# Kernel tuning notes

Measured on AMD Instinct MI355X. Metric: run time of the kernel, lower is better.

The kernel has to match this reference:

```python
import jax, jax.numpy as jnp
import numpy as np

NEG = -1.0e9  # masked_fill value from the original module

def setup_inputs() -> dict:
    key = jax.random.key(0)
    kq, kk, kv, km = jax.random.split(key, 4)
    B, H, S, D = 4, 16, 2048, 64
    Q = jax.random.normal(kq, (B, H, S, D), dtype=jnp.float32)
    K = jax.random.normal(kk, (B, H, S, D), dtype=jnp.float32)
    V = jax.random.normal(kv, (B, H, S, D), dtype=jnp.float32)
    # boolean mask, True = masked out (broadcast over batch and heads)
    mask = jax.random.randint(km, (1, 1, S, S), 0, 2).astype(jnp.bool_)
    return {"Q": Q, "K": K, "V": V, "mask": mask}

def reference(Q, K, V, mask):
    d_k = K.shape[-1]
    scale = 1.0 / jnp.sqrt(jnp.asarray(d_k, dtype=Q.dtype))
    # [B,H,S,S] attention scores
    scores = jnp.einsum("bhqd,bhkd->bhqk", Q, K) * scale
    scores = jnp.where(mask, jnp.asarray(NEG, dtype=scores.dtype), scores)
    weights = jax.nn.softmax(scores, axis=-1)
    # dropout is identity in eval mode (self.training == False)
    return jnp.einsum("bhqk,bhkd->bhqd", weights, V)
```

## Files before the change

kernel.cpp:

```cpp
#include <hip/hip_runtime.h>
#include <stdint.h>

#define SQ 2048
#define DH 64

typedef __attribute__((ext_vector_type(8))) short bf16x8;
typedef __attribute__((ext_vector_type(4))) short bf16x4;
typedef __attribute__((ext_vector_type(4))) float f32x4;

static __device__ __forceinline__ unsigned short f2bf_rne(float x) {
  union { float f; uint32_t u; } v; v.f = x;
  uint32_t u = v.u;
  return (unsigned short)((u + 0x7FFFu + ((u >> 16) & 1u)) >> 16);
}

static __device__ __forceinline__ uint32_t pack_hi(float a, float b) {
  uint32_t au = __float_as_uint(a), bu = __float_as_uint(b);
#if __has_builtin(__builtin_amdgcn_perm)
  return __builtin_amdgcn_perm(bu, au, 0x07060302u);
#else
  return (bu & 0xFFFF0000u) | (au >> 16);
#endif
}

static __device__ __forceinline__ uint32_t pack_sel(float a, float b, uint32_t sel) {
#if __has_builtin(__builtin_amdgcn_perm)
  return __builtin_amdgcn_perm(__float_as_uint(b), __float_as_uint(a), sel);
#else
  uint32_t r = 0;
  uint64_t src = ((uint64_t)__float_as_uint(b) << 32) | __float_as_uint(a);
  for (int i = 0; i < 4; ++i) {
    uint32_t sb = (sel >> (8 * i)) & 0xFF;
    uint32_t byte = (sb < 8) ? (uint32_t)((src >> (8 * sb)) & 0xFF) : 0u;
    r |= byte << (8 * i);
  }
  return r;
#endif
}

static __device__ __forceinline__ float fast_exp2(float x) {
#if __has_builtin(__builtin_amdgcn_exp2f)
  return __builtin_amdgcn_exp2f(x);
#else
  return exp2f(x);
#endif
}

#if __has_builtin(__builtin_amdgcn_mfma_f32_16x16x16_bf16)
#define MFMA_PV(a, b, c) __builtin_amdgcn_mfma_f32_16x16x16_bf16((a), (b), (c), 0, 0, 0)
#else
#define MFMA_PV(a, b, c) __builtin_amdgcn_mfma_f32_16x16x16bf16_1k((a), (b), (c), 0, 0, 0)
#endif

__global__ __launch_bounds__(256) void pack_all(const float* __restrict__ K,
                                                const float* __restrict__ V,
                                                const int* __restrict__ mask,
                                                uint4* __restrict__ pk,
                                                uint2* __restrict__ pv,
                                                uint2* __restrict__ pm) {
  const int t = threadIdx.x;
  if (blockIdx.x < 2048) {
    __shared__ uint32_t Vw[64][33];
    const int bt = blockIdx.x;
    {
      const float* src = K + (size_t)bt * 64 * DH;
      uint4* dst = pk + (size_t)bt * 512;
#pragma unroll
      for (int j = 0; j < 2; ++j) {
        int i = t + j * 256;
        int kk = i >> 3, cp = i & 7;
        int c = cp ^ (kk & 7);
        const float4* s4 = (const float4*)(src + (size_t)kk * DH + c * 8);
        float4 a = s4[0], b = s4[1];
        uint4 w;
        w.x = pack_hi(a.x, a.y); w.y = pack_hi(a.z, a.w);
        w.z = pack_hi(b.x, b.y); w.w = pack_hi(b.z, b.w);
        dst[i] = w;
      }
    }
    {
      const float* src = V + (size_t)bt * 64 * DH;
#pragma unroll
      for (int half = 0; half < 2; ++half) {
        int kp = (t >> 4) + half * 16;
        int d4 = (t & 15) * 4;
        float4 a = *(const float4*)(src + (size_t)(2 * kp) * DH + d4);
        float4 b = *(const float4*)(src + (size_t)(2 * kp + 1) * DH + d4);
        Vw[d4 + 0][kp] = pack_hi(a.x, b.x);
        Vw[d4 + 1][kp] = pack_hi(a.y, b.y);
        Vw[d4 + 2][kp] = pack_hi(a.z, b.z);
        Vw[d4 + 3][kp] = pack_hi(a.w, b.w);
      }
      __syncthreads();
      uint2* dst = pv + (size_t)bt * 1024;
#pragma unroll
      for (int j = 0; j < 4; ++j) {
        int o = t + j * 256;
        int d = o >> 4, up = o & 15;
        int u = up ^ (d & 15);
        uint2 w;
        w.x = Vw[d][2 * u]; w.y = Vw[d][2 * u + 1];
        dst[o] = w;
      }
    }
  } else {
    __shared__ uint2 Lm[16][17];
    const int bid = blockIdx.x - 2048;
    const int qb = bid >> 5, gb = bid & 31;
    {
      int qq = t >> 4, gg = t & 15;
      int4 m = *(const int4*)(mask + (size_t)(qb * 16 + qq) * SQ + (gb * 64 + gg * 4));
      uint2 w;
      w.x = (m.x ? 0x00000C0Cu : 0x00000302u) | (m.y ? 0x0C0C0000u : 0x07060000u);
      w.y = (m.z ? 0x00000C0Cu : 0x00000302u) | (m.w ? 0x0C0C0000u : 0x07060000u);
      Lm[gg][qq] = w;
    }
    __syncthreads();
    {
      int gg = t >> 4, qq = t & 15;
      pm[(size_t)(gb * 16 + gg) * 2048 + qb * 16 + qq] = Lm[gg][qq];
    }
  }
}

__global__ void pack_mask_kernel(const int* __restrict__ mask,
                                 unsigned long long* __restrict__ bits) {
  const int lane = threadIdx.x & 63;
  const int gw = (blockIdx.x * blockDim.x + threadIdx.x) >> 6;
  const int nw = (gridDim.x * blockDim.x) >> 6;
  for (int w = gw; w < SQ * SQ / 64; w += nw) {
    int v = mask[(size_t)w * 64 + lane];
    unsigned long long b = __ballot(v != 0);
    if (lane == 0) bits[(size_t)(w & 31) * SQ + (w >> 5)] = b;
  }
}

__global__ __launch_bounds__(256, 2) void attn3(
    const uint4* __restrict__ pk, const uint4* __restrict__ pv,
    const uint2* __restrict__ pm, const float* __restrict__ Qg,
    float* __restrict__ Og) {
  __shared__ __align__(16) uint8_t smem[32768];

  const int id = blockIdx.x;
  const int bh = id & 63;
  const int qblk = id >> 6;
  const int t = threadIdx.x;
  const int wave = t >> 6, lane = t & 63, col = lane & 15, quad = lane >> 4;

  const float* Qb = Qg + (size_t)bh * SQ * DH;
  float* Ob = Og + (size_t)bh * SQ * DH;
  const uint4* pkb = pk + (size_t)bh * 32 * 512;
  const uint4* pvb = pv + (size_t)bh * 32 * 512;
  const int q0 = qblk * 256 + wave * 64;

  const float QSCALE = 0.18033688011112042f;
  bf16x8 qf[4][2];
#pragma unroll
  for (int s = 0; s < 4; ++s) {
    int q = q0 + s * 16 + col;
#pragma unroll
    for (int j = 0; j < 2; ++j) {
      const float4* p = (const float4*)(Qb + (size_t)q * DH + j * 32 + quad * 8);
      float4 a = p[0], b = p[1];
      bf16x8 f;
      f[0] = (short)f2bf_rne(a.x * QSCALE); f[1] = (short)f2bf_rne(a.y * QSCALE);
      f[2] = (short)f2bf_rne(a.z * QSCALE); f[3] = (short)f2bf_rne(a.w * QSCALE);
      f[4] = (short)f2bf_rne(b.x * QSCALE); f[5] = (short)f2bf_rne(b.y * QSCALE);
      f[6] = (short)f2bf_rne(b.z * QSCALE); f[7] = (short)f2bf_rne(b.w * QSCALE);
      qf[s][j] = f;
    }
  }

  const unsigned ka0 = col * 128 + ((quad ^ (col & 7)) * 16);
  const unsigned ka1 = col * 128 + (((4 + quad) ^ (col & 7)) * 16);
  unsigned va[4];
#pragma unroll
  for (int kt = 0; kt < 4; ++kt)
    va[kt] = 16384u + col * 128 + (((kt * 4 + quad) ^ col) * 8);
  const unsigned stK = t * 16;
  const unsigned stV = 16384u + t * 16;
  const char* pmt = (const char*)pm + (size_t)(quad * 2048 + q0 + col) * 8;

  f32x4 acc[4][4];
  f32x4 accl[4];
#pragma unroll
  for (int s = 0; s < 4; ++s) {
#pragma unroll
    for (int dt = 0; dt < 4; ++dt)
#pragma unroll
      for (int r = 0; r < 4; ++r) acc[s][dt][r] = 0.0f;
#pragma unroll
    for (int r = 0; r < 4; ++r) accl[s][r] = 0.0f;
  }
  bf16x4 vones;
  vones[0] = (short)0x3F80; vones[1] = (short)0x3F80;
  vones[2] = (short)0x3F80; vones[3] = (short)0x3F80;
  const f32x4 fz = {0.0f, 0.0f, 0.0f, 0.0f};

  {
    uint4 k0 = pkb[t], k1 = pkb[t + 256];
    uint4 v0 = pvb[t], v1 = pvb[t + 256];
    *(uint4*)(smem + stK) = k0; *(uint4*)(smem + stK + 4096) = k1;
    *(uint4*)(smem + stV) = v0; *(uint4*)(smem + stV + 4096) = v1;
  }
  unsigned buf = 0;

  for (int tile = 0; tile < 32; ++tile) {
    __syncthreads();
    const int tn = (tile < 31) ? tile + 1 : 31;

    const uint4* pkt = pkb + (size_t)tn * 512;
    const uint4* pvt = pvb + (size_t)tn * 512;
    uint4 k0 = pkt[t], k1 = pkt[t + 256];
    uint4 v0 = pvt[t], v1 = pvt[t + 256];

#pragma unroll
    for (int kt = 0; kt < 4; ++kt) {
      const bf16x8 kf0 = *(const bf16x8*)(smem + buf + kt * 2048 + ka0);
      const bf16x8 kf1 = *(const bf16x8*)(smem + buf + kt * 2048 + ka1);
      uint2 mw[4];
#pragma unroll
      for (int s = 0; s < 4; ++s)
        mw[s] = *(const uint2*)(pmt + (size_t)kt * 65536 + s * 128);

      uint32_t pf[4][2];
#pragma unroll
      for (int s = 0; s < 4; ++s) {
        f32x4 st = __builtin_amdgcn_mfma_f32_16x16x32_bf16(kf0, qf[s][0], fz, 0, 0, 0);
        st = __builtin_amdgcn_mfma_f32_16x16x32_bf16(kf1, qf[s][1], st, 0, 0, 0);
        float p0 = fast_exp2(st[0]), p1 = fast_exp2(st[1]);
        float p2 = fast_exp2(st[2]), p3 = fast_exp2(st[3]);
        pf[s][0] = pack_sel(p0, p1, mw[s].x);
        pf[s][1] = pack_sel(p2, p3, mw[s].y);
      }

      union { uint2 u2; bf16x4 v; } vf[4];
#pragma unroll
      for (int dt = 0; dt < 4; ++dt)
        vf[dt].u2 = *(const uint2*)(smem + buf + va[kt] + dt * 2048);
#pragma unroll
      for (int s = 0; s < 4; ++s) {
        union { uint32_t u[2]; bf16x4 v; } pw;
        pw.u[0] = pf[s][0]; pw.u[1] = pf[s][1];
        accl[s] = MFMA_PV(vones, pw.v, accl[s]);
#pragma unroll
        for (int dt = 0; dt < 4; ++dt)
          acc[s][dt] = MFMA_PV(vf[dt].v, pw.v, acc[s][dt]);
      }
    }

    const unsigned ob = buf ^ 8192u;
    *(uint4*)(smem + ob + stK) = k0; *(uint4*)(smem + ob + stK + 4096) = k1;
    *(uint4*)(smem + ob + stV) = v0; *(uint4*)(smem + ob + stV + 4096) = v1;
    buf = ob;
    pmt += 262144;
  }

#pragma unroll
  for (int s = 0; s < 4; ++s) {
    float inv = 1.0f / accl[s][0];
    int q = q0 + s * 16 + col;
    float* orow = Ob + (size_t)q * DH;
#pragma unroll
    for (int dt = 0; dt < 4; ++dt) {
      float4 o;
      o.x = acc[s][dt][0] * inv;
      o.y = acc[s][dt][1] * inv;
      o.z = acc[s][dt][2] * inv;
      o.w = acc[s][dt][3] * inv;
      *(float4*)(orow + dt * 16 + quad * 4) = o;
    }
  }
}

__global__ __launch_bounds__(512, 4) void attn_fb(
    const float* __restrict__ Qg, const float* __restrict__ Kg,
    const float* __restrict__ Vg, const unsigned long long* __restrict__ mbits,
    const int* __restrict__ mraw, float* __restrict__ Og) {
  __shared__ __align__(16) unsigned short Klds[2][64][72];
  __shared__ __align__(16) uint32_t Vtlds[2][64][36];
  const int id = blockIdx.x;
  const int bh = id & 63;
  const int qblk = id >> 6;
  const int t = threadIdx.x;
  const int wave = t >> 6, lane = t & 63, col = lane & 15, quad = lane >> 4;
  const float* Qb = Qg + (size_t)bh * SQ * DH;
  const float* Kb = Kg + (size_t)bh * SQ * DH;
  const float* Vb = Vg + (size_t)bh * SQ * DH;
  float* Ob = Og + (size_t)bh * SQ * DH;
  const int q0 = qblk * 256 + wave * 32;
  const int skk = t >> 3, sd8 = (t & 7) * 8, skp = t >> 4, sd4 = (t & 15) * 4;
  const float QSCALE = 0.18033688011112042f;
  bf16x8 qf[2][2];
#pragma unroll
  for (int s = 0; s < 2; ++s) {
    int q = q0 + s * 16 + col;
#pragma unroll
    for (int j = 0; j < 2; ++j) {
      const float4* p = (const float4*)(Qb + (size_t)q * DH + j * 32 + quad * 8);
      float4 a = p[0], b = p[1];
      bf16x8 f;
      f[0] = (short)f2bf_rne(a.x * QSCALE); f[1] = (short)f2bf_rne(a.y * QSCALE);
      f[2] = (short)f2bf_rne(a.z * QSCALE); f[3] = (short)f2bf_rne(a.w * QSCALE);
      f[4] = (short)f2bf_rne(b.x * QSCALE); f[5] = (short)f2bf_rne(b.y * QSCALE);
      f[6] = (short)f2bf_rne(b.z * QSCALE); f[7] = (short)f2bf_rne(b.w * QSCALE);
      qf[s][j] = f;
    }
  }
  f32x4 acc[2][4]; f32x4 accl[2];
#pragma unroll
  for (int s = 0; s < 2; ++s) {
#pragma unroll
    for (int dt = 0; dt < 4; ++dt)
#pragma unroll
      for (int r = 0; r < 4; ++r) acc[s][dt][r] = 0.0f;
#pragma unroll
    for (int r = 0; r < 4; ++r) accl[s][r] = 0.0f;
  }
  bf16x4 vones;
  vones[0] = (short)0x3F80; vones[1] = (short)0x3F80;
  vones[2] = (short)0x3F80; vones[3] = (short)0x3F80;
  const f32x4 fz = {0.0f, 0.0f, 0.0f, 0.0f};
  auto load_mask = [&](int ti, unsigned long long m[2]) {
    if (mbits) {
#pragma unroll
      for (int s = 0; s < 2; ++s)
        m[s] = mbits[(size_t)ti * SQ + (q0 + s * 16 + col)];
    } else {
#pragma unroll
      for (int s = 0; s < 2; ++s) {
        int q = q0 + s * 16 + col;
        unsigned long long mm = 0;
#pragma unroll
        for (int j = 0; j < 4; ++j) {
          int4 mi = *(const int4*)(mraw + (size_t)q * SQ + ti * 64 + j * 16 + quad * 4);
          unsigned long long nib = (unsigned long long)((mi.x != 0) | ((mi.y != 0) << 1) |
                                                        ((mi.z != 0) << 2) | ((mi.w != 0) << 3));
          mm |= nib << (j * 16 + quad * 4);
        }
        m[s] = mm;
      }
    }
  };
  {
    const float4* kp = (const float4*)(Kb + (size_t)skk * DH + sd8);
    float4 k0 = kp[0], k1 = kp[1];
    const float* va = Vb + (size_t)(skp * 2) * DH + sd4;
    float4 v0 = *(const float4*)va, v1 = *(const float4*)(va + DH);
    uint4 kw;
    kw.x = pack_hi(k0.x, k0.y); kw.y = pack_hi(k0.z, k0.w);
    kw.z = pack_hi(k1.x, k1.y); kw.w = pack_hi(k1.z, k1.w);
    *(uint4*)&Klds[0][skk][sd8] = kw;
    Vtlds[0][sd4 + 0][skp] = pack_hi(v0.x, v1.x);
    Vtlds[0][sd4 + 1][skp] = pack_hi(v0.y, v1.y);
    Vtlds[0][sd4 + 2][skp] = pack_hi(v0.z, v1.z);
    Vtlds[0][sd4 + 3][skp] = pack_hi(v0.w, v1.w);
  }
  unsigned long long mcur[2];
  load_mask(0, mcur);
  for (int tile = 0; tile < 32; ++tile) {
    __syncthreads();
    const int cb = tile & 1, nb = cb ^ 1;
    const int tn = (tile + 1 < 32) ? tile + 1 : tile;
    const int kkn = tn * 64;
    const float4* kp = (const float4*)(Kb + (size_t)(kkn + skk) * DH + sd8);
    float4 k0 = kp[0], k1 = kp[1];
    const float* va = Vb + (size_t)(kkn + skp * 2) * DH + sd4;
    float4 v0 = *(const float4*)va;
    float4 v1 = *(const float4*)(va + DH);
    unsigned long long mnxt[2];
    load_mask(tn, mnxt);
    uint32_t pfw[2][4][2];
#pragma unroll
    for (int kt = 0; kt < 4; ++kt) {
      const bf16x8 kf0 = *(const bf16x8*)&Klds[cb][kt * 16 + col][quad * 8];
      const bf16x8 kf1 = *(const bf16x8*)&Klds[cb][kt * 16 + col][32 + quad * 8];
#pragma unroll
      for (int s = 0; s < 2; ++s) {
        f32x4 st = __builtin_amdgcn_mfma_f32_16x16x32_bf16(kf0, qf[s][0], fz, 0, 0, 0);
        st = __builtin_amdgcn_mfma_f32_16x16x32_bf16(kf1, qf[s][1], st, 0, 0, 0);
        uint32_t nib = (uint32_t)(mcur[s] >> (kt * 16 + quad * 4)) & 0xFu;
        float p[4];
#pragma unroll
        for (int r = 0; r < 4; ++r)
          p[r] = fast_exp2(((nib >> r) & 1u) ? -1.0e9f : st[r]);
        pfw[s][kt][0] = pack_hi(p[0], p[1]);
        pfw[s][kt][1] = pack_hi(p[2], p[3]);
      }
    }
    {
      uint4 kw;
      kw.x = pack_hi(k0.x, k0.y); kw.y = pack_hi(k0.z, k0.w);
      kw.z = pack_hi(k1.x, k1.y); kw.w = pack_hi(k1.z, k1.w);
      *(uint4*)&Klds[nb][skk][sd8] = kw;
      Vtlds[nb][sd4 + 0][skp] = pack_hi(v0.x, v1.x);
      Vtlds[nb][sd4 + 1][skp] = pack_hi(v0.y, v1.y);
      Vtlds[nb][sd4 + 2][skp] = pack_hi(v0.z, v1.z);
      Vtlds[nb][sd4 + 3][skp] = pack_hi(v0.w, v1.w);
    }
    mcur[0] = mnxt[0]; mcur[1] = mnxt[1];
#pragma unroll
    for (int kt = 0; kt < 4; ++kt) {
      union { uint32_t u[2]; bf16x4 v; } p0, p1;
      p0.u[0] = pfw[0][kt][0]; p0.u[1] = pfw[0][kt][1];
      p1.u[0] = pfw[1][kt][0]; p1.u[1] = pfw[1][kt][1];
      accl[0] = MFMA_PV(vones, p0.v, accl[0]);
      accl[1] = MFMA_PV(vones, p1.v, accl[1]);
#pragma unroll
      for (int dt = 0; dt < 4; ++dt) {
        union { uint2 u2; bf16x4 v; } cv;
        cv.u2 = *(const uint2*)&Vtlds[cb][dt * 16 + col][kt * 8 + quad * 2];
        acc[0][dt] = MFMA_PV(cv.v, p0.v, acc[0][dt]);
        acc[1][dt] = MFMA_PV(cv.v, p1.v, acc[1][dt]);
      }
    }
  }
#pragma unroll
  for (int s = 0; s < 2; ++s) {
    float inv = 1.0f / accl[s][0];
    int q = q0 + s * 16 + col;
    float* orow = Ob + (size_t)q * DH;
#pragma unroll
    for (int dt = 0; dt < 4; ++dt) {
      float4 o;
      o.x = acc[s][dt][0] * inv;
      o.y = acc[s][dt][1] * inv;
      o.z = acc[s][dt][2] * inv;
      o.w = acc[s][dt][3] * inv;
      *(float4*)(orow + dt * 16 + quad * 4) = o;
    }
  }
}

extern "C" void kernel_launch(void* const* d_in, const int* in_sizes, int n_in,
                              void* d_out, int out_size, void* d_ws, size_t ws_size,
                              hipStream_t stream) {
  const float* Q = (const float*)d_in[0];
  const float* K = (const float*)d_in[1];
  const float* V = (const float*)d_in[2];
  const int* mask = (const int*)d_in[3];
  float* out = (float*)d_out;

  const size_t PK_BYTES = (size_t)64 * 32 * 8192;
  const size_t PV_BYTES = (size_t)64 * 32 * 8192;
  const size_t PM_BYTES = (size_t)512 * 2048 * 8;
  const size_t NEED = PK_BYTES + PV_BYTES + PM_BYTES;

  if (ws_size >= NEED) {
    uint4* pk = (uint4*)d_ws;
    uint2* pv = (uint2*)((char*)d_ws + PK_BYTES);
    uint2* pm = (uint2*)((char*)d_ws + PK_BYTES + PV_BYTES);
    pack_all<<<6144, 256, 0, stream>>>(K, V, mask, pk, pv, pm);
    attn3<<<512, 256, 0, stream>>>(pk, (uint4*)pv, pm, Q, out);
  } else if (ws_size >= (size_t)SQ * SQ / 8) {
    unsigned long long* bits = (unsigned long long*)d_ws;
    pack_mask_kernel<<<1024, 256, 0, stream>>>(mask, bits);
    attn_fb<<<512, 512, 0, stream>>>(Q, K, V, bits, mask, out);
  } else {
    attn_fb<<<512, 512, 0, stream>>>(Q, K, V, nullptr, mask, out);
  }
}
```

Before: 242.7 us.

## Split KV dimension across blocks, use direct global-to-LDS loads and 16x16x32 PV MFMA

The attention kernel now splits the 32 key tiles into two halves, launching 1024 blocks instead of 512. Each block writes unnormalised partial outputs and row sums, and a new norm kernel combines the two halves. K, V and mask packing is re-permuted so the PV product can use the 16x16x32 bf16 MFMA with 8-wide fragments. K/V tiles are staged with global_load_lds instead of going through registers. The split aims at better CU occupancy and latency hiding, at the cost of extra partial-result traffic and a third kernel launch.

```diff
diff --git a/kernel.cpp b/kernel.cpp
--- a/kernel.cpp
+++ b/kernel.cpp
@@ -3,6 +3,7 @@
 
 #define SQ 2048
 #define DH 64
+#define BH 64
 
 typedef __attribute__((ext_vector_type(8))) short bf16x8;
 typedef __attribute__((ext_vector_type(4))) short bf16x4;
@@ -46,17 +47,29 @@
 #endif
 }
 
+#define MFMA32(a, b, c) __builtin_amdgcn_mfma_f32_16x16x32_bf16((a), (b), (c), 0, 0, 0)
 #if __has_builtin(__builtin_amdgcn_mfma_f32_16x16x16_bf16)
-#define MFMA_PV(a, b, c) __builtin_amdgcn_mfma_f32_16x16x16_bf16((a), (b), (c), 0, 0, 0)
+#define MFMA_PV16(a, b, c) __builtin_amdgcn_mfma_f32_16x16x16_bf16((a), (b), (c), 0, 0, 0)
 #else
-#define MFMA_PV(a, b, c) __builtin_amdgcn_mfma_f32_16x16x16bf16_1k((a), (b), (c), 0, 0, 0)
+#define MFMA_PV16(a, b, c) __builtin_amdgcn_mfma_f32_16x16x16bf16_1k((a), (b), (c), 0, 0, 0)
 #endif
+
+static __device__ __forceinline__ void stage16(const uint8_t* g, uint8_t* l) {
+#if __has_builtin(__builtin_amdgcn_global_load_lds)
+  __builtin_amdgcn_global_load_lds(
+      (const __attribute__((address_space(1))) uint32_t*)g,
+      (__attribute__((address_space(3))) uint32_t*)l, 16, 0, 0);
+#else
+  *(uint4*)l = *(const uint4*)g;
+#endif
+}
+
 
 __global__ __launch_bounds__(256) void pack_all(const float* __restrict__ K,
                                                 const float* __restrict__ V,
                                                 const int* __restrict__ mask,
                                                 uint4* __restrict__ pk,
-                                                uint2* __restrict__ pv,
+                                                uint4* __restrict__ pv,
                                                 uint2* __restrict__ pm) {
   const int t = threadIdx.x;
   if (blockIdx.x < 2048) {
@@ -68,9 +81,10 @@
 #pragma unroll
       for (int j = 0; j < 2; ++j) {
         int i = t + j * 256;
-        int kk = i >> 3, cp = i & 7;
-        int c = cp ^ (kk & 7);
-        const float4* s4 = (const float4*)(src + (size_t)kk * DH + c * 8);
+        int p = i >> 3, cp = i & 7;
+        int c = cp ^ (p & 7);
+        int lkk = (p & 0x20) | ((p & 0x0C) << 1) | ((p & 0x10) >> 2) | (p & 3);
+        const float4* s4 = (const float4*)(src + (size_t)lkk * DH + c * 8);
         float4 a = s4[0], b = s4[1];
         uint4 w;
         w.x = pack_hi(a.x, a.y); w.y = pack_hi(a.z, a.w);
@@ -92,14 +106,15 @@
         Vw[d4 + 3][kp] = pack_hi(a.w, b.w);
       }
       __syncthreads();
-      uint2* dst = pv + (size_t)bt * 1024;
-#pragma unroll
-      for (int j = 0; j < 4; ++j) {
+      uint4* dst = pv + (size_t)bt * 512;
+#pragma unroll
+      for (int j = 0; j < 2; ++j) {
         int o = t + j * 256;
-        int d = o >> 4, up = o & 15;
-        int u = up ^ (d & 15);
-        uint2 w;
-        w.x = Vw[d][2 * u]; w.y = Vw[d][2 * u + 1];
+        int d = o >> 3, cp = o & 7;
+        int c = cp ^ (d & 7);
+        uint4 w;
+        w.x = Vw[d][4 * c + 0]; w.y = Vw[d][4 * c + 1];
+        w.z = Vw[d][4 * c + 2]; w.w = Vw[d][4 * c + 3];
         dst[o] = w;
       }
     }
@@ -109,7 +124,8 @@
     const int qb = bid >> 5, gb = bid & 31;
     {
       int qq = t >> 4, gg = t & 15;
-      int4 m = *(const int4*)(mask + (size_t)(qb * 16 + qq) * SQ + (gb * 64 + gg * 4));
+      int off = ((gg >> 3) << 5) | ((gg & 3) << 3) | (gg & 4);
+      int4 m = *(const int4*)(mask + (size_t)(qb * 16 + qq) * SQ + gb * 64 + off);
       uint2 w;
       w.x = (m.x ? 0x00000C0Cu : 0x00000302u) | (m.y ? 0x0C0C0000u : 0x07060000u);
       w.y = (m.z ? 0x00000C0Cu : 0x00000302u) | (m.w ? 0x0C0C0000u : 0x07060000u);
@@ -135,22 +151,23 @@
   }
 }
 
-__global__ __launch_bounds__(256, 2) void attn3(
-    const uint4* __restrict__ pk, const uint4* __restrict__ pv,
+__global__ __launch_bounds__(256, 2) void attn4(
+    const uint8_t* __restrict__ pk, const uint8_t* __restrict__ pv,
     const uint2* __restrict__ pm, const float* __restrict__ Qg,
-    float* __restrict__ Og) {
+    float* __restrict__ opart, float* __restrict__ lpart, int ntiles) {
   __shared__ __align__(16) uint8_t smem[32768];
 
   const int id = blockIdx.x;
   const int bh = id & 63;
-  const int qblk = id >> 6;
+  const int qblk = (id >> 6) & 7;
+  const int split = id >> 9;
+  const int tile0 = split * ntiles;
   const int t = threadIdx.x;
   const int wave = t >> 6, lane = t & 63, col = lane & 15, quad = lane >> 4;
 
   const float* Qb = Qg + (size_t)bh * SQ * DH;
-  float* Ob = Og + (size_t)bh * SQ * DH;
-  const uint4* pkb = pk + (size_t)bh * 32 * 512;
-  const uint4* pvb = pv + (size_t)bh * 32 * 512;
+  const uint8_t* pkb = pk + ((size_t)bh * 32 + tile0) * 8192;
+  const uint8_t* pvb = pv + ((size_t)bh * 32 + tile0) * 8192;
   const int q0 = qblk * 256 + wave * 64;
 
   const float QSCALE = 0.18033688011112042f;
@@ -173,13 +190,13 @@
 
   const unsigned ka0 = col * 128 + ((quad ^ (col & 7)) * 16);
   const unsigned ka1 = col * 128 + (((4 + quad) ^ (col & 7)) * 16);
-  unsigned va[4];
-#pragma unroll
-  for (int kt = 0; kt < 4; ++kt)
-    va[kt] = 16384u + col * 128 + (((kt * 4 + quad) ^ col) * 8);
-  const unsigned stK = t * 16;
-  const unsigned stV = 16384u + t * 16;
-  const char* pmt = (const char*)pm + (size_t)(quad * 2048 + q0 + col) * 8;
+  unsigned va[2];
+#pragma unroll
+  for (int ktp = 0; ktp < 2; ++ktp)
+    va[ktp] = 16384u + col * 128 + (((ktp * 4 + quad) ^ (col & 7)) * 16);
+  const unsigned stOff = (unsigned)t * 16;
+  const char* pmt = (const char*)pm +
+                    ((size_t)(tile0 * 16 + quad) * 2048 + q0 + col) * 8;
 
   f32x4 acc[4][4];
   f32x4 accl[4];
@@ -192,84 +209,117 @@
 #pragma unroll
     for (int r = 0; r < 4; ++r) accl[s][r] = 0.0f;
   }
-  bf16x4 vones;
-  vones[0] = (short)0x3F80; vones[1] = (short)0x3F80;
-  vones[2] = (short)0x3F80; vones[3] = (short)0x3F80;
+  bf16x8 vones8;
+#pragma unroll
+  for (int i = 0; i < 8; ++i) vones8[i] = (short)0x3F80;
   const f32x4 fz = {0.0f, 0.0f, 0.0f, 0.0f};
 
-  {
-    uint4 k0 = pkb[t], k1 = pkb[t + 256];
-    uint4 v0 = pvb[t], v1 = pvb[t + 256];
-    *(uint4*)(smem + stK) = k0; *(uint4*)(smem + stK + 4096) = k1;
-    *(uint4*)(smem + stV) = v0; *(uint4*)(smem + stV + 4096) = v1;
-  }
+  stage16(pkb + stOff, smem + stOff);
+  stage16(pkb + 4096 + stOff, smem + 4096 + stOff);
+  stage16(pvb + stOff, smem + 16384 + stOff);
+  stage16(pvb + 4096 + stOff, smem + 20480 + stOff);
   unsigned buf = 0;
 
-  for (int tile = 0; tile < 32; ++tile) {
+  for (int tt = 0; tt < ntiles; ++tt) {
     __syncthreads();
-    const int tn = (tile < 31) ? tile + 1 : 31;
-
-    const uint4* pkt = pkb + (size_t)tn * 512;
-    const uint4* pvt = pvb + (size_t)tn * 512;
-    uint4 k0 = pkt[t], k1 = pkt[t + 256];
-    uint4 v0 = pvt[t], v1 = pvt[t + 256];
-
-#pragma unroll
-    for (int kt = 0; kt < 4; ++kt) {
-      const bf16x8 kf0 = *(const bf16x8*)(smem + buf + kt * 2048 + ka0);
-      const bf16x8 kf1 = *(const bf16x8*)(smem + buf + kt * 2048 + ka1);
-      uint2 mw[4];
-#pragma unroll
-      for (int s = 0; s < 4; ++s)
-        mw[s] = *(const uint2*)(pmt + (size_t)kt * 65536 + s * 128);
-
-      uint32_t pf[4][2];
+    const int tl = (tt + 1 < ntiles) ? tt + 1 : tt;
+    const uint8_t* pkt = pkb + (size_t)tl * 8192;
+    const uint8_t* pvt = pvb + (size_t)tl * 8192;
+    const unsigned ob = buf ^ 8192u;
+    stage16(pkt + stOff, smem + ob + stOff);
+    stage16(pkt + 4096 + stOff, smem + ob + 4096 + stOff);
+    stage16(pvt + stOff, smem + 16384 + ob + stOff);
+    stage16(pvt + 4096 + stOff, smem + 16384 + ob + 4096 + stOff);
+
+    const char* pmc = pmt + (size_t)tt * 262144;
+#pragma unroll
+    for (int ktp = 0; ktp < 2; ++ktp) {
+      uint32_t pf[4][2][2];
+#pragma unroll
+      for (int kh = 0; kh < 2; ++kh) {
+        const int kt = ktp * 2 + kh;
+        const bf16x8 kf0 = *(const bf16x8*)(smem + buf + kt * 2048 + ka0);
+        const bf16x8 kf1 = *(const bf16x8*)(smem + buf + kt * 2048 + ka1);
+        uint2 mw[4];
+#pragma unroll
+        for (int s = 0; s < 4; ++s)
+          mw[s] = *(const uint2*)(pmc + (size_t)kt * 65536 + s * 128);
+#pragma unroll
+        for (int s = 0; s < 4; ++s) {
+          f32x4 st = MFMA32(kf0, qf[s][0], fz);
+          st = MFMA32(kf1, qf[s][1], st);
+          float p0 = fast_exp2(st[0]), p1 = fast_exp2(st[1]);
+          float p2 = fast_exp2(st[2]), p3 = fast_exp2(st[3]);
+          pf[s][kh][0] = pack_sel(p0, p1, mw[s].x);
+          pf[s][kh][1] = pack_sel(p2, p3, mw[s].y);
+        }
+      }
+      union { uint4 u; bf16x8 v; } vf[4];
+#pragma unroll
+      for (int dt = 0; dt < 4; ++dt)
+        vf[dt].u = *(const uint4*)(smem + buf + dt * 2048 + va[ktp]);
 #pragma unroll
       for (int s = 0; s < 4; ++s) {
-        f32x4 st = __builtin_amdgcn_mfma_f32_16x16x32_bf16(kf0, qf[s][0], fz, 0, 0, 0);
-        st = __builtin_amdgcn_mfma_f32_16x16x32_bf16(kf1, qf[s][1], st, 0, 0, 0);
-        float p0 = fast_exp2(st[0]), p1 = fast_exp2(st[1]);
-        float p2 = fast_exp2(st[2]), p3 = fast_exp2(st[3]);
-        pf[s][0] = pack_sel(p0, p1, mw[s].x);
-        pf[s][1] = pack_sel(p2, p3, mw[s].y);
-      }
-
-      union { uint2 u2; bf16x4 v; } vf[4];
-#pragma unroll
-      for (int dt = 0; dt < 4; ++dt)
-        vf[dt].u2 = *(const uint2*)(smem + buf + va[kt] + dt * 2048);
-#pragma unroll
-      for (int s = 0; s < 4; ++s) {
-        union { uint32_t u[2]; bf16x4 v; } pw;
-        pw.u[0] = pf[s][0]; pw.u[1] = pf[s][1];
-        accl[s] = MFMA_PV(vones, pw.v, accl[s]);
+        union { uint32_t u[4]; bf16x8 v; } pw;
+        pw.u[0] = pf[s][0][0]; pw.u[1] = pf[s][0][1];
+        pw.u[2] = pf[s][1][0]; pw.u[3] = pf[s][1][1];
+        accl[s] = MFMA32(vones8, pw.v, accl[s]);
 #pragma unroll
         for (int dt = 0; dt < 4; ++dt)
-          acc[s][dt] = MFMA_PV(vf[dt].v, pw.v, acc[s][dt]);
-      }
-    }
-
-    const unsigned ob = buf ^ 8192u;
-    *(uint4*)(smem + ob + stK) = k0; *(uint4*)(smem + ob + stK + 4096) = k1;
-    *(uint4*)(smem + ob + stV) = v0; *(uint4*)(smem + ob + stV + 4096) = v1;
+          acc[s][dt] = MFMA32(vf[dt].v, pw.v, acc[s][dt]);
+      }
+    }
     buf = ob;
-    pmt += 262144;
-  }
-
-#pragma unroll
-  for (int s = 0; s < 4; ++s) {
-    float inv = 1.0f / accl[s][0];
-    int q = q0 + s * 16 + col;
-    float* orow = Ob + (size_t)q * DH;
-#pragma unroll
-    for (int dt = 0; dt < 4; ++dt) {
-      float4 o;
-      o.x = acc[s][dt][0] * inv;
-      o.y = acc[s][dt][1] * inv;
-      o.z = acc[s][dt][2] * inv;
-      o.w = acc[s][dt][3] * inv;
-      *(float4*)(orow + dt * 16 + quad * 4) = o;
-    }
+  }
+
+  if (lpart) {
+    float* obase = opart + ((size_t)split * BH + bh) * SQ * DH;
+    float* lbase = lpart + (size_t)split * BH * SQ + (size_t)bh * SQ;
+#pragma unroll
+    for (int s = 0; s < 4; ++s) {
+      int q = q0 + s * 16 + col;
+      float* orow = obase + (size_t)q * DH;
+#pragma unroll
+      for (int dt = 0; dt < 4; ++dt) {
+        float4 o;
+        o.x = acc[s][dt][0]; o.y = acc[s][dt][1];
+        o.z = acc[s][dt][2]; o.w = acc[s][dt][3];
+        *(float4*)(orow + dt * 16 + quad * 4) = o;
+      }
+      if (quad == 0) lbase[q] = accl[s][0];
+    }
+  } else {
+    float* obase = opart + (size_t)bh * SQ * DH;
+#pragma unroll
+    for (int s = 0; s < 4; ++s) {
+      float inv = 1.0f / accl[s][0];
+      int q = q0 + s * 16 + col;
+      float* orow = obase + (size_t)q * DH;
+#pragma unroll
+      for (int dt = 0; dt < 4; ++dt) {
+        float4 o;
+        o.x = acc[s][dt][0] * inv; o.y = acc[s][dt][1] * inv;
+        o.z = acc[s][dt][2] * inv; o.w = acc[s][dt][3] * inv;
+        *(float4*)(orow + dt * 16 + quad * 4) = o;
+      }
+    }
+  }
+}
+
+__global__ __launch_bounds__(256) void norm_kernel(const float4* __restrict__ p,
+                                                   const float* __restrict__ l,
+                                                   float4* __restrict__ out) {
+  const size_t N4 = (size_t)BH * SQ * DH / 4;
+  size_t i = (size_t)blockIdx.x * 256 + threadIdx.x;
+  const size_t stride = (size_t)gridDim.x * 256;
+  for (; i < N4; i += stride) {
+    size_t ql = i >> 4;
+    float inv = 1.0f / (l[ql] + l[(size_t)BH * SQ + ql]);
+    float4 a = p[i], b = p[N4 + i];
+    float4 o;
+    o.x = (a.x + b.x) * inv; o.y = (a.y + b.y) * inv;
+    o.z = (a.z + b.z) * inv; o.w = (a.w + b.w) * inv;
+    out[i] = o;
   }
 }
 
@@ -377,8 +427,8 @@
       const bf16x8 kf1 = *(const bf16x8*)&Klds[cb][kt * 16 + col][32 + quad * 8];
 #pragma unroll
       for (int s = 0; s < 2; ++s) {
-        f32x4 st = __builtin_amdgcn_mfma_f32_16x16x32_bf16(kf0, qf[s][0], fz, 0, 0, 0);
-        st = __builtin_amdgcn_mfma_f32_16x16x32_bf16(kf1, qf[s][1], st, 0, 0, 0);
+        f32x4 st = MFMA32(kf0, qf[s][0], fz);
+        st = MFMA32(kf1, qf[s][1], st);
         uint32_t nib = (uint32_t)(mcur[s] >> (kt * 16 + quad * 4)) & 0xFu;
         float p[4];
 #pragma unroll
@@ -404,14 +454,14 @@
       union { uint32_t u[2]; bf16x4 v; } p0, p1;
       p0.u[0] = pfw[0][kt][0]; p0.u[1] = pfw[0][kt][1];
       p1.u[0] = pfw[1][kt][0]; p1.u[1] = pfw[1][kt][1];
-      accl[0] = MFMA_PV(vones, p0.v, accl[0]);
-      accl[1] = MFMA_PV(vones, p1.v, accl[1]);
+      accl[0] = MFMA_PV16(vones, p0.v, accl[0]);
+      accl[1] = MFMA_PV16(vones, p1.v, accl[1]);
 #pragma unroll
       for (int dt = 0; dt < 4; ++dt) {
         union { uint2 u2; bf16x4 v; } cv;
         cv.u2 = *(const uint2*)&Vtlds[cb][dt * 16 + col][kt * 8 + quad * 2];
-        acc[0][dt] = MFMA_PV(cv.v, p0.v, acc[0][dt]);
-        acc[1][dt] = MFMA_PV(cv.v, p1.v, acc[1][dt]);
+        acc[0][dt] = MFMA_PV16(cv.v, p0.v, acc[0][dt]);
+        acc[1][dt] = MFMA_PV16(cv.v, p1.v, acc[1][dt]);
       }
     }
   }
@@ -441,17 +491,30 @@
   const int* mask = (const int*)d_in[3];
   float* out = (float*)d_out;
 
-  const size_t PK_BYTES = (size_t)64 * 32 * 8192;
-  const size_t PV_BYTES = (size_t)64 * 32 * 8192;
+  const size_t PK_BYTES = (size_t)BH * 32 * 8192;
+  const size_t PV_BYTES = (size_t)BH * 32 * 8192;
   const size_t PM_BYTES = (size_t)512 * 2048 * 8;
-  const size_t NEED = PK_BYTES + PV_BYTES + PM_BYTES;
-
-  if (ws_size >= NEED) {
+  const size_t NEED_PACK = PK_BYTES + PV_BYTES + PM_BYTES;
+  const size_t OP_BYTES = (size_t)2 * BH * SQ * DH * 4;
+  const size_t LP_BYTES = (size_t)2 * BH * SQ * 4;
+  const size_t NEED_SPLIT = NEED_PACK + OP_BYTES + LP_BYTES;
+
+  if (ws_size >= NEED_PACK) {
     uint4* pk = (uint4*)d_ws;
-    uint2* pv = (uint2*)((char*)d_ws + PK_BYTES);
+    uint4* pv = (uint4*)((char*)d_ws + PK_BYTES);
     uint2* pm = (uint2*)((char*)d_ws + PK_BYTES + PV_BYTES);
     pack_all<<<6144, 256, 0, stream>>>(K, V, mask, pk, pv, pm);
-    attn3<<<512, 256, 0, stream>>>(pk, (uint4*)pv, pm, Q, out);
+    if (ws_size >= NEED_SPLIT) {
+      float* opart = (float*)((char*)d_ws + NEED_PACK);
+      float* lpart = (float*)((char*)d_ws + NEED_PACK + OP_BYTES);
+      attn4<<<1024, 256, 0, stream>>>((const uint8_t*)pk, (const uint8_t*)pv, pm,
+                                      Q, opart, lpart, 16);
+      norm_kernel<<<4096, 256, 0, stream>>>((const float4*)opart, lpart,
+                                            (float4*)out);
+    } else {
+      attn4<<<512, 256, 0, stream>>>((const uint8_t*)pk, (const uint8_t*)pv, pm,
+                                     Q, out, nullptr, 32);
+    }
   } else if (ws_size >= (size_t)SQ * SQ / 8) {
     unsigned long long* bits = (unsigned long long*)d_ws;
     pack_mask_kernel<<<1024, 256, 0, stream>>>(mask, bits);
```

Result: slower. 261.1 us (+7.6%).
